# Kernel optimization log

Measured on AMD Instinct MI355X. Metric: run time of the kernel, lower is better.

Reference implementation:

```python
import jax, jax.numpy as jnp
import numpy as np

T, N, E, F, H = 8, 50000, 800000, 128, 128
NHEADS = 4
DH = H // NHEADS


def setup_inputs() -> dict:
    key = jax.random.key(0)
    ks = jax.random.split(key, 24)

    def rn(k, shape, scale=0.05):
        return jax.random.normal(k, shape, dtype=jnp.float32) * scale

    return {
        "xs": rn(ks[0], (T, N, F), 1.0),
        "edge_index": jax.random.randint(ks[1], (T, 2, E), 0, N, dtype=jnp.int32),
        # SAGEConv layers: out = mean_aggr(x_src) @ Wl + x @ Wr + b (bias on lin_l only)
        "Wl1": rn(ks[2], (F, H)), "Wr1": rn(ks[3], (F, H)), "b1": jnp.zeros((H,), jnp.float32),
        "Wl2": rn(ks[4], (H, H)), "Wr2": rn(ks[5], (H, H)), "b2": jnp.zeros((H,), jnp.float32),
        "Wl3": rn(ks[6], (H, H)), "Wr3": rn(ks[7], (H, H)), "b3": jnp.zeros((H,), jnp.float32),
        # MultiheadAttention (applied as x @ W, i.e. W = torch_weight.T)
        "Wq": rn(ks[8], (H, H)), "bq": jnp.zeros((H,), jnp.float32),
        "Wk": rn(ks[9], (H, H)), "bk": jnp.zeros((H,), jnp.float32),
        "Wv": rn(ks[10], (H, H)), "bv": jnp.zeros((H,), jnp.float32),
        "Wo": rn(ks[11], (H, H)), "bo": jnp.zeros((H,), jnp.float32),
        # MLP head
        "Wh1": rn(ks[12], (H, H // 2)), "bh1": jnp.zeros((H // 2,), jnp.float32),
        "Wh2": rn(ks[13], (H // 2, 1)), "bh2": jnp.zeros((1,), jnp.float32),
    }


def _sage(x, src, dst, Wl, Wr, b):
    # gather messages from source nodes, mean-aggregate at destinations
    msg = x[src]                                               # [E, F]
    ssum = jax.ops.segment_sum(msg, dst, num_segments=N)       # [N, F]
    cnt = jax.ops.segment_sum(jnp.ones((msg.shape[0],), x.dtype), dst, num_segments=N)
    agg = ssum / jnp.maximum(cnt, 1.0)[:, None]
    return agg @ Wl + x @ Wr + b


def reference(xs, edge_index, Wl1, Wr1, b1, Wl2, Wr2, b2, Wl3, Wr3, b3,
              Wq, bq, Wk, bk, Wv, bv, Wo, bo, Wh1, bh1, Wh2, bh2):
    def step(_, xe):
        x, ei = xe
        src, dst = ei[0], ei[1]
        h = jax.nn.relu(_sage(x, src, dst, Wl1, Wr1, b1))  # dropout = identity (eval)
        h = jax.nn.relu(_sage(h, src, dst, Wl2, Wr2, b2))
        h = jax.nn.relu(_sage(h, src, dst, Wl3, Wr3, b3))
        return None, h.mean(axis=0)                        # mean pool over nodes -> [H]

    _, pooled = jax.lax.scan(step, None, (xs, edge_index))  # [T, H]

    seq = pooled[None]                                      # [1, T, H]
    q = (seq @ Wq + bq).reshape(1, T, NHEADS, DH).transpose(0, 2, 1, 3)
    k = (seq @ Wk + bk).reshape(1, T, NHEADS, DH).transpose(0, 2, 1, 3)
    v = (seq @ Wv + bv).reshape(1, T, NHEADS, DH).transpose(0, 2, 1, 3)
    scale = jnp.float32(1.0 / np.sqrt(DH))
    attn = jax.nn.softmax(jnp.einsum('bhqd,bhkd->bhqk', q, k) * scale, axis=-1)
    o = jnp.einsum('bhqk,bhkd->bhqd', attn, v).transpose(0, 2, 1, 3).reshape(1, T, H)
    o = o @ Wo + bo                                         # [1, T, H]

    z = o[:, -1, :]                                         # [1, H] (last timestep)
    h1 = jax.nn.relu(z @ Wh1 + bh1)
    logits = jax.nn.sigmoid(h1 @ Wh2 + bh2)                 # [1, 1]
    return logits.squeeze(-1)                               # [1]
```

## Files before the change

### kernel.cpp

```cpp
#include <hip/hip_runtime.h>
#include <math.h>

#define TT 8
#define NN 50000
#define EE 800000
#define FF 128
#define HH 128

#define NB 98
#define BSHIFT 9
#define CAP 14336
#define RS 16384

typedef __attribute__((ext_vector_type(8))) short short8;
typedef __attribute__((ext_vector_type(4))) float f32x4;
typedef __attribute__((ext_vector_type(2))) float f32x2;
typedef unsigned char uchar;

__device__ inline unsigned bf16pack(float x) {
    unsigned u = __float_as_uint(x);
    return (u + 0x7fffu + ((u >> 16) & 1u)) >> 16;
}
__device__ inline unsigned pack2bf16_trunc(float lo, float hi) {
    return (__float_as_uint(hi) & 0xffff0000u) | (__float_as_uint(lo) >> 16);
}


__global__ __launch_bounds__(256) void cast_x_kernel(const float4* __restrict__ in,
                                                     int* __restrict__ out, long n4) {
    long i = (long)blockIdx.x * 256 + threadIdx.x;
    if (i < n4) {
        float4 v = in[i];
        int w = __builtin_amdgcn_cvt_pk_fp8_f32(v.x, v.y, 0, false);
        w = __builtin_amdgcn_cvt_pk_fp8_f32(v.z, v.w, w, true);
        out[i] = w;
    }
}

__global__ __launch_bounds__(256) void wprep_kernel(const float* __restrict__ Wl1, const float* __restrict__ Wr1,
                                                    const float* __restrict__ Wl2, const float* __restrict__ Wr2,
                                                    const float* __restrict__ Wl3, const float* __restrict__ Wr3,
                                                    ushort* __restrict__ Bt1, ushort* __restrict__ Bt2,
                                                    ushort* __restrict__ Bt3) {
    int which = blockIdx.y;
    const float* Wl = (which == 0) ? Wl1 : (which == 1) ? Wl2 : Wl3;
    const float* Wr = (which == 0) ? Wr1 : (which == 1) ? Wr2 : Wr3;
    ushort* Bt = (which == 0) ? Bt1 : (which == 1) ? Bt2 : Bt3;
    int n = blockIdx.x;
    int k = threadIdx.x;
    float v = (k < 128) ? Wl[k * HH + n] : Wr[(k - 128) * HH + n];
    Bt[n * 256 + k] = (ushort)bf16pack(v);
}


__global__ __launch_bounds__(256) void partA_kernel(const int* __restrict__ ei,
                                                    int* __restrict__ bucketCursor,
                                                    uint2* __restrict__ pairs) {
    __shared__ int hist[NB];
    __shared__ int base[NB];
    int t = blockIdx.y, tid = threadIdx.x;
    const int* src = ei + (size_t)t * 2 * EE;
    const int* dst = src + EE;
    int e0 = blockIdx.x * 2048;
    int s[8], d[8];
#pragma unroll
    for (int k = 0; k < 8; k++) {
        int e = e0 + k * 256 + tid;
        bool ok = e < EE;
        s[k] = ok ? src[e] : -1;
        d[k] = ok ? dst[e] : -1;
    }
    if (tid < NB) hist[tid] = 0;
    __syncthreads();
#pragma unroll
    for (int k = 0; k < 8; k++)
        if (d[k] >= 0) atomicAdd(&hist[d[k] >> BSHIFT], 1);
    __syncthreads();
    if (tid < NB) {
        base[tid] = atomicAdd(&bucketCursor[t * NB + tid], hist[tid]);
        hist[tid] = 0;
    }
    __syncthreads();
#pragma unroll
    for (int k = 0; k < 8; k++)
        if (d[k] >= 0) {
            int b = d[k] >> BSHIFT;
            int idx = base[b] + atomicAdd(&hist[b], 1);
            if (idx < CAP)
                pairs[((size_t)t * NB + b) * RS + idx] = make_uint2((unsigned)s[k], (unsigned)d[k]);
        }
}

__global__ void bscan_kernel(const int* __restrict__ bucketCursor,
                             int* __restrict__ bucketBase) {
    int t = threadIdx.x;
    if (t < TT) {
        int run = 0;
        for (int b = 0; b < NB; b++) {
            bucketBase[t * NB + b] = run;
            int c = bucketCursor[t * NB + b];
            run += (c > CAP ? CAP : c);
        }
    }
}

__global__ __launch_bounds__(256) void partB_kernel(const uint2* __restrict__ pairs,
                                                    const int* __restrict__ bucketCursor,
                                                    const int* __restrict__ bucketBase,
                                                    int* __restrict__ cnt,
                                                    int* __restrict__ rowstart,
                                                    int* __restrict__ srcs_sorted) {
    __shared__ int hist[512];
    __shared__ int offs[512];
    __shared__ int sh2[256];
    __shared__ int staged[CAP];
    int t = blockIdx.y, b = blockIdx.x, tid = threadIdx.x;
    int n0 = b << BSHIFT;
    int nn = NN - n0; if (nn > 512) nn = 512;
    int cb = bucketCursor[t * NB + b]; if (cb > CAP) cb = CAP;
    int ebase = bucketBase[t * NB + b];
    const uint2* P = pairs + ((size_t)t * NB + b) * RS;

    hist[tid] = 0; hist[tid + 256] = 0;
    __syncthreads();
    for (int i = tid; i < cb; i += 256) atomicAdd(&hist[(int)P[i].y - n0], 1);
    __syncthreads();
    int a0 = hist[2 * tid], a1 = hist[2 * tid + 1];
    sh2[tid] = a0 + a1;
    __syncthreads();
    for (int off = 1; off < 256; off <<= 1) {
        int v = (tid >= off) ? sh2[tid - off] : 0;
        __syncthreads();
        sh2[tid] += v;
        __syncthreads();
    }
    int excl = sh2[tid] - (a0 + a1);
    offs[2 * tid] = excl;
    offs[2 * tid + 1] = excl + a0;
    __syncthreads();
    for (int i = tid; i < nn; i += 256) {
        cnt[(size_t)t * NN + n0 + i] = hist[i];
        rowstart[(size_t)t * NN + n0 + i] = ebase + offs[i];
    }
    __syncthreads();
    hist[tid] = offs[tid]; hist[tid + 256] = offs[tid + 256];
    __syncthreads();
    for (int i = tid; i < cb; i += 256) {
        uint2 p = P[i];
        int slot = atomicAdd(&hist[(int)p.y - n0], 1);
        staged[slot] = (int)p.x;
    }
    __syncthreads();
    int* outp = srcs_sorted + (size_t)t * EE + ebase;
    for (int i = tid; i < cb; i += 256) outp[i] = staged[i];
}

#define ACCP(V)                                                          \
    do {                                                                 \
        A0 += __builtin_amdgcn_cvt_pk_f32_fp8((int)(V).x, false);        \
        A1 += __builtin_amdgcn_cvt_pk_f32_fp8((int)(V).x, true);         \
        A2 += __builtin_amdgcn_cvt_pk_f32_fp8((int)(V).y, false);        \
        A3 += __builtin_amdgcn_cvt_pk_f32_fp8((int)(V).y, true);         \
    } while (0)

__global__ __launch_bounds__(256) void agg_kernel(const uchar* __restrict__ xinF,
                                                  const int* __restrict__ srcs_sortedF,
                                                  const int* __restrict__ rowstartF,
                                                  const int* __restrict__ cntF,
                                                  uchar* __restrict__ aggqF) {
    int t = blockIdx.y;
    int node = blockIdx.x * 4 + (threadIdx.x >> 6);
    if (node >= NN) return;
    int lane = threadIdx.x & 63;
    int quad = lane >> 4;
    unsigned lby = (unsigned)((lane & 15) << 3);

    const char* xb = (const char*)xinF + (size_t)t * NN * HH;
    const int* srcs = srcs_sortedF + (size_t)t * EE;
    char* ob = (char*)aggqF + (size_t)t * NN * HH;

    int rs = rowstartF[t * NN + node];
    int c = cntF[t * NN + node];

    f32x2 A0 = (f32x2){0.f, 0.f}, A1 = A0, A2 = A0, A3 = A0;
    int j = quad;
    for (; j + 12 < c; j += 16) {
        int i0 = srcs[rs + j];
        int i1 = srcs[rs + j + 4];
        int i2 = srcs[rs + j + 8];
        int i3 = srcs[rs + j + 12];
        uint2 v0 = *(const uint2*)(xb + (((unsigned)i0 << 7) | lby));
        uint2 v1 = *(const uint2*)(xb + (((unsigned)i1 << 7) | lby));
        uint2 v2 = *(const uint2*)(xb + (((unsigned)i2 << 7) | lby));
        uint2 v3 = *(const uint2*)(xb + (((unsigned)i3 << 7) | lby));
        ACCP(v0); ACCP(v1); ACCP(v2); ACCP(v3);
    }
    if (j + 4 < c) {
        int i0 = srcs[rs + j];
        int i1 = srcs[rs + j + 4];
        uint2 v0 = *(const uint2*)(xb + (((unsigned)i0 << 7) | lby));
        uint2 v1 = *(const uint2*)(xb + (((unsigned)i1 << 7) | lby));
        ACCP(v0); ACCP(v1);
        j += 8;
    }
    if (j < c) {
        int i0 = srcs[rs + j];
        uint2 v0 = *(const uint2*)(xb + (((unsigned)i0 << 7) | lby));
        ACCP(v0);
    }
#pragma unroll
    for (int o = 16; o <= 32; o <<= 1) {
        f32x2 B0, B1, B2, B3;
        B0.x = __shfl_xor(A0.x, o, 64); B0.y = __shfl_xor(A0.y, o, 64);
        B1.x = __shfl_xor(A1.x, o, 64); B1.y = __shfl_xor(A1.y, o, 64);
        B2.x = __shfl_xor(A2.x, o, 64); B2.y = __shfl_xor(A2.y, o, 64);
        B3.x = __shfl_xor(A3.x, o, 64); B3.y = __shfl_xor(A3.y, o, 64);
        A0 += B0; A1 += B1; A2 += B2; A3 += B3;
    }
    if (quad == 0) {
        float inv = 1.0f / (float)(c > 0 ? c : 1);
        int w0 = __builtin_amdgcn_cvt_pk_fp8_f32(A0.x * inv, A0.y * inv, 0, false);
        w0 = __builtin_amdgcn_cvt_pk_fp8_f32(A1.x * inv, A1.y * inv, w0, true);
        int w1 = __builtin_amdgcn_cvt_pk_fp8_f32(A2.x * inv, A2.y * inv, 0, false);
        w1 = __builtin_amdgcn_cvt_pk_fp8_f32(A3.x * inv, A3.y * inv, w1, true);
        *(uint2*)(ob + (((unsigned)node << 7) | lby)) = make_uint2((unsigned)w0, (unsigned)w1);
    }
}

template <int POOL>
__global__ __launch_bounds__(256) void gemm_mfma_kernel(const uchar* __restrict__ AaggF,
                                                        const uchar* __restrict__ AxF,
                                                        const ushort* __restrict__ Bt,
                                                        const float* __restrict__ bias,
                                                        uchar* __restrict__ outF,
                                                        float* __restrict__ pooled) {
    extern __shared__ char smem[];
    ushort* As = (ushort*)smem;
    ushort* Bs = (ushort*)(smem + 128 * 72 * 2);
    uchar* Cs = (uchar*)smem;

    size_t toff = (size_t)blockIdx.y * NN * HH;
    const uchar* Aagg = AaggF + toff;
    const uchar* Ax = AxF + toff;
    uchar* out = outF + toff;

    int tid = threadIdx.x;
    int row0 = blockIdx.x * 128;
    int lane = tid & 63, wave = tid >> 6;
    int wm = wave >> 1, wn = wave & 1;
    int l15 = lane & 15, quad = lane >> 4;

    f32x4 acc[4][4];
#pragma unroll
    for (int i = 0; i < 4; i++)
#pragma unroll
        for (int j = 0; j < 4; j++) acc[i][j] = (f32x4){0.f, 0.f, 0.f, 0.f};

    int srow = tid >> 1;
    int cb = (tid & 1) * 32;
    int grow = row0 + srow;

    uint4 r0 = make_uint4(0u, 0u, 0u, 0u), r1 = r0;
    if (grow < NN) {
        const uchar* ap = Aagg + (size_t)grow * HH + cb;
        r0 = *(const uint4*)ap;
        r1 = *(const uint4*)(ap + 16);
    }

    for (int s = 0; s < 4; s++) {
        unsigned w[8] = {r0.x, r0.y, r0.z, r0.w, r1.x, r1.y, r1.z, r1.w};
        unsigned u[16];
#pragma unroll
        for (int wi = 0; wi < 8; wi++) {
            f32x2 lo = __builtin_amdgcn_cvt_pk_f32_fp8((int)w[wi], false);
            f32x2 hi = __builtin_amdgcn_cvt_pk_f32_fp8((int)w[wi], true);
            u[2 * wi] = pack2bf16_trunc(lo.x, lo.y);
            u[2 * wi + 1] = pack2bf16_trunc(hi.x, hi.y);
        }
        const ushort* bp = Bt + srow * 256 + s * 64 + cb;
        uint4 bv[4];
#pragma unroll
        for (int c = 0; c < 4; c++) bv[c] = *(const uint4*)(bp + c * 8);
        __syncthreads();
#pragma unroll
        for (int c = 0; c < 4; c++)
            *(uint4*)&As[srow * 72 + cb + c * 8] =
                make_uint4(u[4 * c], u[4 * c + 1], u[4 * c + 2], u[4 * c + 3]);
#pragma unroll
        for (int c = 0; c < 4; c++) *(uint4*)&Bs[srow * 72 + cb + c * 8] = bv[c];
        __syncthreads();
        if (s < 3) {
            const uchar* Asrc = (s + 1 < 2) ? Aagg : Ax;
            int acol = ((s + 1) & 1) * 64 + cb;
            r0 = make_uint4(0u, 0u, 0u, 0u);
            r1 = r0;
            if (grow < NN) {
                const uchar* ap = Asrc + (size_t)grow * HH + acol;
                r0 = *(const uint4*)ap;
                r1 = *(const uint4*)(ap + 16);
            }
        }
#pragma unroll
        for (int ks = 0; ks < 2; ks++) {
            int k0 = ks * 32 + quad * 8;
            short8 a[4], b[4];
#pragma unroll
            for (int i = 0; i < 4; i++)
                a[i] = *(const short8*)&As[(wm * 64 + i * 16 + l15) * 72 + k0];
#pragma unroll
            for (int j = 0; j < 4; j++)
                b[j] = *(const short8*)&Bs[(wn * 64 + j * 16 + l15) * 72 + k0];
#pragma unroll
            for (int i = 0; i < 4; i++)
#pragma unroll
                for (int j = 0; j < 4; j++)
                    acc[i][j] = __builtin_amdgcn_mfma_f32_16x16x32_bf16(a[i], b[j], acc[i][j], 0, 0, 0);
        }
    }
    __syncthreads();

    if (POOL == 0) {
#pragma unroll
        for (int i = 0; i < 4; i++)
#pragma unroll
            for (int j = 0; j < 4; j++) {
                int col = wn * 64 + j * 16 + l15;
                float bb = bias[col];
#pragma unroll
                for (int r = 0; r < 4; r++) {
                    int rl = wm * 64 + i * 16 + quad * 4 + r;
                    float v = fmaxf(acc[i][j][r] + bb, 0.f);
                    int pk = __builtin_amdgcn_cvt_pk_fp8_f32(v, 0.f, 0, false);
                    Cs[rl * 144 + col] = (uchar)(pk & 0xff);
                }
            }
        __syncthreads();

        int orow = tid >> 1;
        int ocb = (tid & 1) * 64;
        if (row0 + orow < NN) {
#pragma unroll
            for (int c = 0; c < 4; c++)
                *(uint4*)&out[(size_t)(row0 + orow) * HH + ocb + c * 16] =
                    *(const uint4*)&Cs[orow * 144 + ocb + c * 16];
        }
    } else {
        float* colsum = (float*)smem;
        if (tid < HH) colsum[tid] = 0.f;
        __syncthreads();
#pragma unroll
        for (int j = 0; j < 4; j++) {
            int col = wn * 64 + j * 16 + l15;
            float bb = bias[col];
            float ps = 0.f;
#pragma unroll
            for (int i = 0; i < 4; i++)
#pragma unroll
                for (int r = 0; r < 4; r++) {
                    int rl = wm * 64 + i * 16 + quad * 4 + r;
                    float v = fmaxf(acc[i][j][r] + bb, 0.f);
                    ps += (row0 + rl < NN) ? v : 0.f;
                }
            ps += __shfl_xor(ps, 16, 64);
            ps += __shfl_xor(ps, 32, 64);
            if (quad == 0) atomicAdd(&colsum[col], ps);
        }
        __syncthreads();
        if (tid < HH)
            atomicAdd(&pooled[blockIdx.y * HH + tid], colsum[tid] * (1.0f / (float)NN));
    }
}

__global__ __launch_bounds__(256) void head_kernel(const float* __restrict__ pooled,
                                                   const float* __restrict__ Wq, const float* __restrict__ bq,
                                                   const float* __restrict__ Wk, const float* __restrict__ bk,
                                                   const float* __restrict__ Wv, const float* __restrict__ bv,
                                                   const float* __restrict__ Wo, const float* __restrict__ bo,
                                                   const float* __restrict__ Wh1, const float* __restrict__ bh1,
                                                   const float* __restrict__ Wh2, const float* __restrict__ bh2,
                                                   float* __restrict__ out) {
    __shared__ float seq[TT * HH];
    __shared__ float kb[TT * HH];
    __shared__ float vbuf[TT * HH];
    __shared__ float q7[HH];
    __shared__ float sc[4][8];
    __shared__ float zb[HH];
    __shared__ float ob[HH];
    __shared__ float h1b[64];
    int tid = threadIdx.x;
    for (int i = tid; i < TT * HH; i += 256) seq[i] = pooled[i];
    __syncthreads();
    for (int i = tid; i < TT * HH; i += 256) {
        int t = i >> 7, h = i & 127;
        float sk = bk[h], sv = bv[h];
        for (int j = 0; j < HH; j++) {
            float s = seq[t * HH + j];
            sk += s * Wk[j * HH + h];
            sv += s * Wv[j * HH + h];
        }
        kb[i] = sk;
        vbuf[i] = sv;
    }
    if (tid < HH) {
        float sq = bq[tid];
        for (int j = 0; j < HH; j++) sq += seq[7 * HH + j] * Wq[j * HH + tid];
        q7[tid] = sq;
    }
    __syncthreads();
    if (tid < 32) {
        int g = tid >> 3, tt = tid & 7;
        float s = 0.f;
        for (int d = 0; d < 32; d++) s += q7[g * 32 + d] * kb[tt * HH + g * 32 + d];
        sc[g][tt] = s * 0.1767766952966369f;
    }
    __syncthreads();
    if (tid < 4) {
        float m = -1e30f;
        for (int i = 0; i < 8; i++) m = fmaxf(m, sc[tid][i]);
        float e[8], sum = 0.f;
        for (int i = 0; i < 8; i++) { e[i] = expf(sc[tid][i] - m); sum += e[i]; }
        for (int i = 0; i < 8; i++) sc[tid][i] = e[i] / sum;
    }
    __syncthreads();
    if (tid < HH) {
        int g = tid >> 5;
        float s = 0.f;
        for (int t = 0; t < 8; t++) s += sc[g][t] * vbuf[t * HH + tid];
        zb[tid] = s;
    }
    __syncthreads();
    if (tid < HH) {
        float s = bo[tid];
        for (int j = 0; j < HH; j++) s += zb[j] * Wo[j * HH + tid];
        ob[tid] = s;
    }
    __syncthreads();
    if (tid < 64) {
        float s = bh1[tid];
        for (int j = 0; j < HH; j++) s += ob[j] * Wh1[j * 64 + tid];
        h1b[tid] = fmaxf(s, 0.f);
    }
    __syncthreads();
    if (tid == 0) {
        float s = bh2[0];
        for (int j = 0; j < 64; j++) s += h1b[j] * Wh2[j];
        out[0] = 1.0f / (1.0f + expf(-s));
    }
}


extern "C" void kernel_launch(void* const* d_in, const int* in_sizes, int n_in,
                              void* d_out, int out_size, void* d_ws, size_t ws_size,
                              hipStream_t stream) {
    const float* xs = (const float*)d_in[0];
    const int* ei = (const int*)d_in[1];
    const float* Wl1 = (const float*)d_in[2];
    const float* Wr1 = (const float*)d_in[3];
    const float* b1 = (const float*)d_in[4];
    const float* Wl2 = (const float*)d_in[5];
    const float* Wr2 = (const float*)d_in[6];
    const float* b2 = (const float*)d_in[7];
    const float* Wl3 = (const float*)d_in[8];
    const float* Wr3 = (const float*)d_in[9];
    const float* b3 = (const float*)d_in[10];
    const float* Wq = (const float*)d_in[11];
    const float* bq = (const float*)d_in[12];
    const float* Wk = (const float*)d_in[13];
    const float* bk = (const float*)d_in[14];
    const float* Wv = (const float*)d_in[15];
    const float* bv = (const float*)d_in[16];
    const float* Wo = (const float*)d_in[17];
    const float* bo = (const float*)d_in[18];
    const float* Wh1 = (const float*)d_in[19];
    const float* bh1 = (const float*)d_in[20];
    const float* Wh2 = (const float*)d_in[21];
    const float* bh2 = (const float*)d_in[22];

    size_t off = 0;
    char* base = (char*)d_ws;
    auto carve = [&](size_t bytes) -> char* {
        char* p = base + off;
        off += (bytes + 255) & ~(size_t)255;
        return p;
    };
    int* cnt = (int*)carve((size_t)TT * NN * 4);
    int* rowstart = (int*)carve((size_t)TT * NN * 4);
    int* srcs_sorted = (int*)carve((size_t)TT * EE * 4);
    int* bucketCursor = (int*)carve((size_t)TT * NB * 4);
    int* bucketBase = (int*)carve((size_t)TT * NB * 4);
    uint2* pairs = (uint2*)carve((size_t)TT * NB * RS * 8);
    uchar* xq = (uchar*)carve((size_t)TT * NN * HH);
    uchar* aggq = (uchar*)carve((size_t)TT * NN * HH);
    uchar* h1q = (uchar*)carve((size_t)TT * NN * HH);
    uchar* h2q = (uchar*)carve((size_t)TT * NN * HH);
    ushort* Bt1 = (ushort*)carve((size_t)128 * 256 * 2);
    ushort* Bt2 = (ushort*)carve((size_t)128 * 256 * 2);
    ushort* Bt3 = (ushort*)carve((size_t)128 * 256 * 2);
    float* pooled = (float*)carve((size_t)TT * HH * 4);

    hipMemsetAsync(pooled, 0, (size_t)TT * HH * 4, stream);
    hipMemsetAsync(bucketCursor, 0, (size_t)TT * NB * 4, stream);

    long n4 = (long)TT * NN * FF / 4;
    cast_x_kernel<<<(int)((n4 + 255) / 256), 256, 0, stream>>>((const float4*)xs, (int*)xq, n4);
    wprep_kernel<<<dim3(128, 3), 256, 0, stream>>>(Wl1, Wr1, Wl2, Wr2, Wl3, Wr3, Bt1, Bt2, Bt3);

    partA_kernel<<<dim3((EE + 2047) / 2048, TT), 256, 0, stream>>>(ei, bucketCursor, pairs);
    bscan_kernel<<<1, 64, 0, stream>>>(bucketCursor, bucketBase);
    partB_kernel<<<dim3(NB, TT), 256, 0, stream>>>(pairs, bucketCursor, bucketBase,
                                                   cnt, rowstart, srcs_sorted);

    const int gemmGrid = (NN + 127) / 128;
    const int aggGrid = (NN + 3) / 4;
    const int gemmLds = 128 * 72 * 2 * 2;

    agg_kernel<<<dim3(aggGrid, TT), 256, 0, stream>>>(xq, srcs_sorted, rowstart, cnt, aggq);
    gemm_mfma_kernel<0><<<dim3(gemmGrid, TT), 256, gemmLds, stream>>>(aggq, xq, Bt1, b1, h1q, nullptr);
    agg_kernel<<<dim3(aggGrid, TT), 256, 0, stream>>>(h1q, srcs_sorted, rowstart, cnt, aggq);
    gemm_mfma_kernel<0><<<dim3(gemmGrid, TT), 256, gemmLds, stream>>>(aggq, h1q, Bt2, b2, h2q, nullptr);
    agg_kernel<<<dim3(aggGrid, TT), 256, 0, stream>>>(h2q, srcs_sorted, rowstart, cnt, aggq);
    gemm_mfma_kernel<1><<<dim3(gemmGrid, TT), 256, gemmLds, stream>>>(aggq, h2q, Bt3, b3, h1q, pooled);

    head_kernel<<<1, 256, 0, stream>>>(pooled, Wq, bq, Wk, bk, Wv, bv, Wo, bo,
                                       Wh1, bh1, Wh2, bh2, (float*)d_out);
}
```

Before: 1.218 ms.

## Fuse neighbor aggregation into MFMA GEMM kernel via LDS-resident bf16 tile

Merges the separate aggregation and GEMM kernels into one kernel per SAGE layer. Each block gathers and mean-aggregates its 128 nodes into an LDS buffer as bf16, then runs the MFMA GEMM reading aggregated rows from LDS. The x-self operand and the weight fragments are read straight from global memory instead of being staged through LDS. This removes the fp8 agg intermediate round trip through HBM and half the launches, but serializes gather latency before the compute within each block. It also uses about 35KB of static LDS, which may lower occupancy for the latency-bound gather phase.

New measurement: 1.630 ms. +33.9%, slower.

```diff
diff --git a/kernel.cpp b/kernel.cpp
--- a/kernel.cpp
+++ b/kernel.cpp
@@ -155,161 +155,154 @@
     for (int i = tid; i < cb; i += 256) outp[i] = staged[i];
 }
 
-#define ACCP(V)                                                          \
-    do {                                                                 \
-        A0 += __builtin_amdgcn_cvt_pk_f32_fp8((int)(V).x, false);        \
-        A1 += __builtin_amdgcn_cvt_pk_f32_fp8((int)(V).x, true);         \
-        A2 += __builtin_amdgcn_cvt_pk_f32_fp8((int)(V).y, false);        \
-        A3 += __builtin_amdgcn_cvt_pk_f32_fp8((int)(V).y, true);         \
-    } while (0)
-
-__global__ __launch_bounds__(256) void agg_kernel(const uchar* __restrict__ xinF,
-                                                  const int* __restrict__ srcs_sortedF,
-                                                  const int* __restrict__ rowstartF,
-                                                  const int* __restrict__ cntF,
-                                                  uchar* __restrict__ aggqF) {
+template <int POOL>
+__global__ __launch_bounds__(256) void fused_agg_gemm_kernel(
+        const uchar* __restrict__ xinF,
+        const int* __restrict__ srcs_sortedF,
+        const int* __restrict__ rowstartF,
+        const int* __restrict__ cntF,
+        const ushort* __restrict__ Bt,
+        const float* __restrict__ bias,
+        uchar* __restrict__ outF,
+        float* __restrict__ pooled) {
+    __shared__ ushort aggbuf[128 * 136];
+
     int t = blockIdx.y;
-    int node = blockIdx.x * 4 + (threadIdx.x >> 6);
-    if (node >= NN) return;
-    int lane = threadIdx.x & 63;
-    int quad = lane >> 4;
-    unsigned lby = (unsigned)((lane & 15) << 3);
-
     const char* xb = (const char*)xinF + (size_t)t * NN * HH;
     const int* srcs = srcs_sortedF + (size_t)t * EE;
-    char* ob = (char*)aggqF + (size_t)t * NN * HH;
-
-    int rs = rowstartF[t * NN + node];
-    int c = cntF[t * NN + node];
-
-    f32x2 A0 = (f32x2){0.f, 0.f}, A1 = A0, A2 = A0, A3 = A0;
-    int j = quad;
-    for (; j + 12 < c; j += 16) {
-        int i0 = srcs[rs + j];
-        int i1 = srcs[rs + j + 4];
-        int i2 = srcs[rs + j + 8];
-        int i3 = srcs[rs + j + 12];
-        uint2 v0 = *(const uint2*)(xb + (((unsigned)i0 << 7) | lby));
-        uint2 v1 = *(const uint2*)(xb + (((unsigned)i1 << 7) | lby));
-        uint2 v2 = *(const uint2*)(xb + (((unsigned)i2 << 7) | lby));
-        uint2 v3 = *(const uint2*)(xb + (((unsigned)i3 << 7) | lby));
-        ACCP(v0); ACCP(v1); ACCP(v2); ACCP(v3);
-    }
-    if (j + 4 < c) {
-        int i0 = srcs[rs + j];
-        int i1 = srcs[rs + j + 4];
-        uint2 v0 = *(const uint2*)(xb + (((unsigned)i0 << 7) | lby));
-        uint2 v1 = *(const uint2*)(xb + (((unsigned)i1 << 7) | lby));
-        ACCP(v0); ACCP(v1);
-        j += 8;
-    }
-    if (j < c) {
-        int i0 = srcs[rs + j];
-        uint2 v0 = *(const uint2*)(xb + (((unsigned)i0 << 7) | lby));
-        ACCP(v0);
-    }
-#pragma unroll
-    for (int o = 16; o <= 32; o <<= 1) {
-        f32x2 B0, B1, B2, B3;
-        B0.x = __shfl_xor(A0.x, o, 64); B0.y = __shfl_xor(A0.y, o, 64);
-        B1.x = __shfl_xor(A1.x, o, 64); B1.y = __shfl_xor(A1.y, o, 64);
-        B2.x = __shfl_xor(A2.x, o, 64); B2.y = __shfl_xor(A2.y, o, 64);
-        B3.x = __shfl_xor(A3.x, o, 64); B3.y = __shfl_xor(A3.y, o, 64);
-        A0 += B0; A1 += B1; A2 += B2; A3 += B3;
-    }
-    if (quad == 0) {
-        float inv = 1.0f / (float)(c > 0 ? c : 1);
-        int w0 = __builtin_amdgcn_cvt_pk_fp8_f32(A0.x * inv, A0.y * inv, 0, false);
-        w0 = __builtin_amdgcn_cvt_pk_fp8_f32(A1.x * inv, A1.y * inv, w0, true);
-        int w1 = __builtin_amdgcn_cvt_pk_fp8_f32(A2.x * inv, A2.y * inv, 0, false);
-        w1 = __builtin_amdgcn_cvt_pk_fp8_f32(A3.x * inv, A3.y * inv, w1, true);
-        *(uint2*)(ob + (((unsigned)node << 7) | lby)) = make_uint2((unsigned)w0, (unsigned)w1);
-    }
-}
-
-template <int POOL>
-__global__ __launch_bounds__(256) void gemm_mfma_kernel(const uchar* __restrict__ AaggF,
-                                                        const uchar* __restrict__ AxF,
-                                                        const ushort* __restrict__ Bt,
-                                                        const float* __restrict__ bias,
-                                                        uchar* __restrict__ outF,
-                                                        float* __restrict__ pooled) {
-    extern __shared__ char smem[];
-    ushort* As = (ushort*)smem;
-    ushort* Bs = (ushort*)(smem + 128 * 72 * 2);
-    uchar* Cs = (uchar*)smem;
-
-    size_t toff = (size_t)blockIdx.y * NN * HH;
-    const uchar* Aagg = AaggF + toff;
-    const uchar* Ax = AxF + toff;
-    uchar* out = outF + toff;
+    const int* rsA = rowstartF + t * NN;
+    const int* cnA = cntF + t * NN;
+    uchar* out = outF + (size_t)t * NN * HH;
 
     int tid = threadIdx.x;
     int row0 = blockIdx.x * 128;
     int lane = tid & 63, wave = tid >> 6;
+    int l15 = lane & 15, quad = lane >> 4;
+    unsigned lby = (unsigned)(l15 << 3);
+
+    for (int it = 0; it < 32; ++it) {
+        int rloc = wave * 32 + it;
+        int node = row0 + rloc;
+        f32x2 A0 = (f32x2){0.f, 0.f}, A1 = A0, A2 = A0, A3 = A0;
+        int c = 0;
+        if (node < NN) {
+            int rs = rsA[node];
+            c = cnA[node];
+            int j = quad;
+            for (; j + 12 < c; j += 16) {
+                int i0 = srcs[rs + j];
+                int i1 = srcs[rs + j + 4];
+                int i2 = srcs[rs + j + 8];
+                int i3 = srcs[rs + j + 12];
+                uint2 v0 = *(const uint2*)(xb + (((unsigned)i0 << 7) | lby));
+                uint2 v1 = *(const uint2*)(xb + (((unsigned)i1 << 7) | lby));
+                uint2 v2 = *(const uint2*)(xb + (((unsigned)i2 << 7) | lby));
+                uint2 v3 = *(const uint2*)(xb + (((unsigned)i3 << 7) | lby));
+                A0 += __builtin_amdgcn_cvt_pk_f32_fp8((int)v0.x, false);
+                A1 += __builtin_amdgcn_cvt_pk_f32_fp8((int)v0.x, true);
+                A2 += __builtin_amdgcn_cvt_pk_f32_fp8((int)v0.y, false);
+                A3 += __builtin_amdgcn_cvt_pk_f32_fp8((int)v0.y, true);
+                A0 += __builtin_amdgcn_cvt_pk_f32_fp8((int)v1.x, false);
+                A1 += __builtin_amdgcn_cvt_pk_f32_fp8((int)v1.x, true);
+                A2 += __builtin_amdgcn_cvt_pk_f32_fp8((int)v1.y, false);
+                A3 += __builtin_amdgcn_cvt_pk_f32_fp8((int)v1.y, true);
+                A0 += __builtin_amdgcn_cvt_pk_f32_fp8((int)v2.x, false);
+                A1 += __builtin_amdgcn_cvt_pk_f32_fp8((int)v2.x, true);
+                A2 += __builtin_amdgcn_cvt_pk_f32_fp8((int)v2.y, false);
+                A3 += __builtin_amdgcn_cvt_pk_f32_fp8((int)v2.y, true);
+                A0 += __builtin_amdgcn_cvt_pk_f32_fp8((int)v3.x, false);
+                A1 += __builtin_amdgcn_cvt_pk_f32_fp8((int)v3.x, true);
+                A2 += __builtin_amdgcn_cvt_pk_f32_fp8((int)v3.y, false);
+                A3 += __builtin_amdgcn_cvt_pk_f32_fp8((int)v3.y, true);
+            }
+            if (j + 4 < c) {
+                int i0 = srcs[rs + j];
+                int i1 = srcs[rs + j + 4];
+                uint2 v0 = *(const uint2*)(xb + (((unsigned)i0 << 7) | lby));
+                uint2 v1 = *(const uint2*)(xb + (((unsigned)i1 << 7) | lby));
+                A0 += __builtin_amdgcn_cvt_pk_f32_fp8((int)v0.x, false);
+                A1 += __builtin_amdgcn_cvt_pk_f32_fp8((int)v0.x, true);
+                A2 += __builtin_amdgcn_cvt_pk_f32_fp8((int)v0.y, false);
+                A3 += __builtin_amdgcn_cvt_pk_f32_fp8((int)v0.y, true);
+                A0 += __builtin_amdgcn_cvt_pk_f32_fp8((int)v1.x, false);
+                A1 += __builtin_amdgcn_cvt_pk_f32_fp8((int)v1.x, true);
+                A2 += __builtin_amdgcn_cvt_pk_f32_fp8((int)v1.y, false);
+                A3 += __builtin_amdgcn_cvt_pk_f32_fp8((int)v1.y, true);
+                j += 8;
+            }
+            if (j < c) {
+                int i0 = srcs[rs + j];
+                uint2 v0 = *(const uint2*)(xb + (((unsigned)i0 << 7) | lby));
+                A0 += __builtin_amdgcn_cvt_pk_f32_fp8((int)v0.x, false);
+                A1 += __builtin_amdgcn_cvt_pk_f32_fp8((int)v0.x, true);
+                A2 += __builtin_amdgcn_cvt_pk_f32_fp8((int)v0.y, false);
+                A3 += __builtin_amdgcn_cvt_pk_f32_fp8((int)v0.y, true);
+            }
+        }
+#pragma unroll
+        for (int o = 16; o <= 32; o <<= 1) {
+            f32x2 B0, B1, B2, B3;
+            B0.x = __shfl_xor(A0.x, o, 64); B0.y = __shfl_xor(A0.y, o, 64);
+            B1.x = __shfl_xor(A1.x, o, 64); B1.y = __shfl_xor(A1.y, o, 64);
+            B2.x = __shfl_xor(A2.x, o, 64); B2.y = __shfl_xor(A2.y, o, 64);
+            B3.x = __shfl_xor(A3.x, o, 64); B3.y = __shfl_xor(A3.y, o, 64);
+            A0 += B0; A1 += B1; A2 += B2; A3 += B3;
+        }
+        if (quad == 0) {
+            float inv = 1.0f / (float)(c > 0 ? c : 1);
+            uint4 w;
+            w.x = bf16pack(A0.x * inv) | (bf16pack(A0.y * inv) << 16);
+            w.y = bf16pack(A1.x * inv) | (bf16pack(A1.y * inv) << 16);
+            w.z = bf16pack(A2.x * inv) | (bf16pack(A2.y * inv) << 16);
+            w.w = bf16pack(A3.x * inv) | (bf16pack(A3.y * inv) << 16);
+            *(uint4*)&aggbuf[rloc * 136 + l15 * 8] = w;
+        }
+    }
+    __syncthreads();
+
     int wm = wave >> 1, wn = wave & 1;
-    int l15 = lane & 15, quad = lane >> 4;
-
     f32x4 acc[4][4];
 #pragma unroll
     for (int i = 0; i < 4; i++)
 #pragma unroll
         for (int j = 0; j < 4; j++) acc[i][j] = (f32x4){0.f, 0.f, 0.f, 0.f};
 
-    int srow = tid >> 1;
-    int cb = (tid & 1) * 32;
-    int grow = row0 + srow;
-
-    uint4 r0 = make_uint4(0u, 0u, 0u, 0u), r1 = r0;
-    if (grow < NN) {
-        const uchar* ap = Aagg + (size_t)grow * HH + cb;
-        r0 = *(const uint4*)ap;
-        r1 = *(const uint4*)(ap + 16);
-    }
-
+    union frag_u { short8 s8; uint4 u4; };
+
+#pragma unroll
     for (int s = 0; s < 4; s++) {
-        unsigned w[8] = {r0.x, r0.y, r0.z, r0.w, r1.x, r1.y, r1.z, r1.w};
-        unsigned u[16];
-#pragma unroll
-        for (int wi = 0; wi < 8; wi++) {
-            f32x2 lo = __builtin_amdgcn_cvt_pk_f32_fp8((int)w[wi], false);
-            f32x2 hi = __builtin_amdgcn_cvt_pk_f32_fp8((int)w[wi], true);
-            u[2 * wi] = pack2bf16_trunc(lo.x, lo.y);
-            u[2 * wi + 1] = pack2bf16_trunc(hi.x, hi.y);
-        }
-        const ushort* bp = Bt + srow * 256 + s * 64 + cb;
-        uint4 bv[4];
-#pragma unroll
-        for (int c = 0; c < 4; c++) bv[c] = *(const uint4*)(bp + c * 8);
-        __syncthreads();
-#pragma unroll
-        for (int c = 0; c < 4; c++)
-            *(uint4*)&As[srow * 72 + cb + c * 8] =
-                make_uint4(u[4 * c], u[4 * c + 1], u[4 * c + 2], u[4 * c + 3]);
-#pragma unroll
-        for (int c = 0; c < 4; c++) *(uint4*)&Bs[srow * 72 + cb + c * 8] = bv[c];
-        __syncthreads();
-        if (s < 3) {
-            const uchar* Asrc = (s + 1 < 2) ? Aagg : Ax;
-            int acol = ((s + 1) & 1) * 64 + cb;
-            r0 = make_uint4(0u, 0u, 0u, 0u);
-            r1 = r0;
-            if (grow < NN) {
-                const uchar* ap = Asrc + (size_t)grow * HH + acol;
-                r0 = *(const uint4*)ap;
-                r1 = *(const uint4*)(ap + 16);
+#pragma unroll
+        for (int ks = 0; ks < 2; ks++) {
+            int kq = ks * 32 + quad * 8;
+            short8 a[4], b[4];
+            if (s < 2) {
+                int kg = s * 64 + kq;
+#pragma unroll
+                for (int i = 0; i < 4; i++)
+                    a[i] = *(const short8*)&aggbuf[(wm * 64 + i * 16 + l15) * 136 + kg];
+            } else {
+                int kg = (s - 2) * 64 + kq;
+#pragma unroll
+                for (int i = 0; i < 4; i++) {
+                    int r = row0 + wm * 64 + i * 16 + l15;
+                    uint2 v = make_uint2(0u, 0u);
+                    if (r < NN) v = *(const uint2*)(xb + (((unsigned)r << 7) + (unsigned)kg));
+                    f32x2 lo0 = __builtin_amdgcn_cvt_pk_f32_fp8((int)v.x, false);
+                    f32x2 hi0 = __builtin_amdgcn_cvt_pk_f32_fp8((int)v.x, true);
+                    f32x2 lo1 = __builtin_amdgcn_cvt_pk_f32_fp8((int)v.y, false);
+                    f32x2 hi1 = __builtin_amdgcn_cvt_pk_f32_fp8((int)v.y, true);
+                    frag_u fu;
+                    fu.u4 = make_uint4(pack2bf16_trunc(lo0.x, lo0.y),
+                                       pack2bf16_trunc(hi0.x, hi0.y),
+                                       pack2bf16_trunc(lo1.x, lo1.y),
+                                       pack2bf16_trunc(hi1.x, hi1.y));
+                    a[i] = fu.s8;
+                }
             }
-        }
-#pragma unroll
-        for (int ks = 0; ks < 2; ks++) {
-            int k0 = ks * 32 + quad * 8;
-            short8 a[4], b[4];
-#pragma unroll
-            for (int i = 0; i < 4; i++)
-                a[i] = *(const short8*)&As[(wm * 64 + i * 16 + l15) * 72 + k0];
+            int kb = s * 64 + kq;
 #pragma unroll
             for (int j = 0; j < 4; j++)
-                b[j] = *(const short8*)&Bs[(wn * 64 + j * 16 + l15) * 72 + k0];
+                b[j] = *(const short8*)&Bt[(wn * 64 + j * 16 + l15) * 256 + kb];
 #pragma unroll
             for (int i = 0; i < 4; i++)
 #pragma unroll
@@ -320,6 +313,7 @@
     __syncthreads();
 
     if (POOL == 0) {
+        uchar* Cs = (uchar*)aggbuf;
 #pragma unroll
         for (int i = 0; i < 4; i++)
 #pragma unroll
@@ -345,7 +339,7 @@
                     *(const uint4*)&Cs[orow * 144 + ocb + c * 16];
         }
     } else {
-        float* colsum = (float*)smem;
+        float* colsum = (float*)aggbuf;
         if (tid < HH) colsum[tid] = 0.f;
         __syncthreads();
 #pragma unroll
@@ -490,7 +484,6 @@
     int* bucketBase = (int*)carve((size_t)TT * NB * 4);
     uint2* pairs = (uint2*)carve((size_t)TT * NB * RS * 8);
     uchar* xq = (uchar*)carve((size_t)TT * NN * HH);
-    uchar* aggq = (uchar*)carve((size_t)TT * NN * HH);
     uchar* h1q = (uchar*)carve((size_t)TT * NN * HH);
     uchar* h2q = (uchar*)carve((size_t)TT * NN * HH);
     ushort* Bt1 = (ushort*)carve((size_t)128 * 256 * 2);
@@ -511,15 +504,13 @@
                                                    cnt, rowstart, srcs_sorted);
 
     const int gemmGrid = (NN + 127) / 128;
-    const int aggGrid = (NN + 3) / 4;
-    const int gemmLds = 128 * 72 * 2 * 2;
-
-    agg_kernel<<<dim3(aggGrid, TT), 256, 0, stream>>>(xq, srcs_sorted, rowstart, cnt, aggq);
-    gemm_mfma_kernel<0><<<dim3(gemmGrid, TT), 256, gemmLds, stream>>>(aggq, xq, Bt1, b1, h1q, nullptr);
-    agg_kernel<<<dim3(aggGrid, TT), 256, 0, stream>>>(h1q, srcs_sorted, rowstart, cnt, aggq);
-    gemm_mfma_kernel<0><<<dim3(gemmGrid, TT), 256, gemmLds, stream>>>(aggq, h1q, Bt2, b2, h2q, nullptr);
-    agg_kernel<<<dim3(aggGrid, TT), 256, 0, stream>>>(h2q, srcs_sorted, rowstart, cnt, aggq);
-    gemm_mfma_kernel<1><<<dim3(gemmGrid, TT), 256, gemmLds, stream>>>(aggq, h2q, Bt3, b3, h1q, pooled);
+
+    fused_agg_gemm_kernel<0><<<dim3(gemmGrid, TT), 256, 0, stream>>>(
+        xq, srcs_sorted, rowstart, cnt, Bt1, b1, h1q, nullptr);
+    fused_agg_gemm_kernel<0><<<dim3(gemmGrid, TT), 256, 0, stream>>>(
+        h1q, srcs_sorted, rowstart, cnt, Bt2, b2, h2q, nullptr);
+    fused_agg_gemm_kernel<1><<<dim3(gemmGrid, TT), 256, 0, stream>>>(
+        h2q, srcs_sorted, rowstart, cnt, Bt3, b3, h1q, pooled);
 
     head_kernel<<<1, 256, 0, stream>>>(pooled, Wq, bq, Wk, bk, Wv, bv, Wo, bo,
                                        Wh1, bh1, Wh2, bh2, (float*)d_out);
```
